# Kernel optimization log

Hardware: AMD Instinct MI355X
Metric: run time of the kernel (lower is better)

Reference implementation:

```python
import jax, jax.numpy as jnp
import numpy as np

MARGIN = 0.2


def _pairwise_distances(emb):
    # Euclidean distances with torch-style zero-masked sqrt (non-squared path).
    dot = jnp.matmul(emb, emb.T)                      # [N, N]
    sq = jnp.diagonal(dot)                            # [N]
    d2 = sq[None, :] - 2.0 * dot + sq[:, None]
    d2 = jnp.maximum(d2, 0.0)
    zero_mask = (d2 == 0.0).astype(d2.dtype)
    return (1.0 - zero_mask) * jnp.sqrt(d2 + zero_mask * 1e-16)


def setup_inputs() -> dict:
    key = jax.random.key(0)
    k1, k2 = jax.random.split(key)
    N, D, C = 512, 512, 64
    labels = jax.random.randint(k1, (N,), 0, C, dtype=jnp.int64 if jax.config.jax_enable_x64 else jnp.int32)
    embeddings = jax.random.normal(k2, (N, D), dtype=jnp.float32)
    return {"labels": labels, "embeddings": embeddings}


def reference(labels, embeddings):
    # Semi-hard... actually Difficulty.Easy path of TripletLoss.forward
    N = embeddings.shape[0]
    pdist = _pairwise_distances(embeddings)                      # [N, N]
    adjacency_not = labels[None, :] != labels[:, None]           # [N, N] bool

    pdist_tile = jnp.tile(pdist, (N, 1))                         # [N*N, N]
    mask = jnp.tile(adjacency_not, (N, 1))                       # [N*N, N]
    # Easy difficulty: negatives strictly farther than the anchor-positive dist
    mask = mask & (pdist_tile > pdist.T.reshape(-1, 1))

    maskf = mask.astype(pdist.dtype)
    mask_final = (jnp.sum(maskf, axis=1, keepdims=True) > 0.0).reshape(N, N).T  # [N, N] bool

    # masked minimum over tiled rows
    axis_max = jnp.max(pdist_tile, axis=1, keepdims=True)
    neg_outside = (jnp.min((pdist_tile - axis_max) * maskf, axis=1, keepdims=True)
                   + axis_max).reshape(N, N).T                   # [N, N]

    # masked maximum over negatives per anchor
    adjf = adjacency_not.astype(pdist.dtype)
    axis_min = jnp.min(pdist, axis=1, keepdims=True)
    neg_inside = jnp.max((pdist - axis_min) * adjf, axis=1, keepdims=True) + axis_min  # [N, 1]
    neg_inside = jnp.broadcast_to(neg_inside, (N, N))

    semi_hard_negatives = jnp.where(mask_final, neg_outside, neg_inside)
    loss_mat = MARGIN + pdist - semi_hard_negatives

    eye = jnp.eye(N, dtype=bool)
    mask_positives = (labels[None, :] == labels[:, None]) & ~eye
    num_positives = jnp.sum(mask_positives).astype(loss_mat.dtype)
    loss = jnp.sum(jnp.maximum(loss_mat * mask_positives.astype(loss_mat.dtype), 0.0))
    return loss / (num_positives + 1e-8)
```

## Files before the change

### kernel.cpp

```cpp
#include <hip/hip_runtime.h>
#include <math.h>


#define NN 512
#define MARGIN_F 0.2f
#define LK 520

typedef __attribute__((ext_vector_type(8))) short bf16x8;
typedef __attribute__((ext_vector_type(4))) float f32x4;

__device__ __forceinline__ unsigned short f2bf(float x){
    unsigned u = __float_as_uint(x);
    return (unsigned short)((u + 0x7FFFu + ((u >> 16) & 1u)) >> 16);
}
__device__ __forceinline__ float bf2f(unsigned short h){
    return __uint_as_float(((unsigned)h) << 16);
}

__global__ __launch_bounds__(256) void k_dist(
    const float* __restrict__ emb,
    float* __restrict__ Dm,
    int* __restrict__ ctrl)
{
    __shared__ __align__(16) char sm[133376];
    short* sh  = (short*)sm;
    float* snI = (float*)(sm + 133120);
    float* snJ = snI + 32;

    const int tid  = threadIdx.x;
    const int wave = tid >> 6, lane = tid & 63;
    const int bi = blockIdx.y, bj = blockIdx.x;

    if (bi == 0 && bj == 0 && tid < 3) ctrl[tid] = 0;

    {
        const int row = tid >> 3;
        const int s8  = tid & 7;
        const float4* Ep = (const float4*)emb;
        float ssI = 0.f, ssJ = 0.f;
        #pragma unroll
        for (int i = 0; i < 16; ++i) {
            const int c4 = s8 + (i << 3);
            const float4 vI = Ep[(size_t)(bi * 32 + row) * 128 + c4];
            const float4 vJ = Ep[(size_t)(bj * 32 + row) * 128 + c4];
            ssI = fmaf(vI.x, vI.x, ssI); ssI = fmaf(vI.y, vI.y, ssI);
            ssI = fmaf(vI.z, vI.z, ssI); ssI = fmaf(vI.w, vI.w, ssI);
            ssJ = fmaf(vJ.x, vJ.x, ssJ); ssJ = fmaf(vJ.y, vJ.y, ssJ);
            ssJ = fmaf(vJ.z, vJ.z, ssJ); ssJ = fmaf(vJ.w, vJ.w, ssJ);
            ushort4 h, l;
            h.x = f2bf(vI.x); l.x = f2bf(vI.x - bf2f(h.x));
            h.y = f2bf(vI.y); l.y = f2bf(vI.y - bf2f(h.y));
            h.z = f2bf(vI.z); l.z = f2bf(vI.z - bf2f(h.z));
            h.w = f2bf(vI.w); l.w = f2bf(vI.w - bf2f(h.w));
            *(ushort4*)(&sh[(0 * 32 + row) * LK + (c4 << 2)]) = h;
            *(ushort4*)(&sh[(1 * 32 + row) * LK + (c4 << 2)]) = l;
            h.x = f2bf(vJ.x); l.x = f2bf(vJ.x - bf2f(h.x));
            h.y = f2bf(vJ.y); l.y = f2bf(vJ.y - bf2f(h.y));
            h.z = f2bf(vJ.z); l.z = f2bf(vJ.z - bf2f(h.z));
            h.w = f2bf(vJ.w); l.w = f2bf(vJ.w - bf2f(h.w));
            *(ushort4*)(&sh[(2 * 32 + row) * LK + (c4 << 2)]) = h;
            *(ushort4*)(&sh[(3 * 32 + row) * LK + (c4 << 2)]) = l;
        }
        ssI += __shfl_xor(ssI, 1, 64); ssJ += __shfl_xor(ssJ, 1, 64);
        ssI += __shfl_xor(ssI, 2, 64); ssJ += __shfl_xor(ssJ, 2, 64);
        ssI += __shfl_xor(ssI, 4, 64); ssJ += __shfl_xor(ssJ, 4, 64);
        if (s8 == 0) { snI[row] = ssI; snJ[row] = ssJ; }
    }
    __syncthreads();

    const int rowb = (wave >> 1) << 4, colb = (wave & 1) << 4;
    const int fr = lane & 15;
    const int k0 = (lane >> 4) << 3;
    f32x4 acc = {0.f, 0.f, 0.f, 0.f};
    #pragma unroll
    for (int t8 = 0; t8 < 16; ++t8) {
        const int k = k0 + (t8 << 5);
        bf16x8 ahi = *(const bf16x8*)(&sh[(0 * 32 + rowb + fr) * LK + k]);
        bf16x8 alo = *(const bf16x8*)(&sh[(1 * 32 + rowb + fr) * LK + k]);
        bf16x8 bhi = *(const bf16x8*)(&sh[(2 * 32 + colb + fr) * LK + k]);
        bf16x8 blo = *(const bf16x8*)(&sh[(3 * 32 + colb + fr) * LK + k]);
        acc = __builtin_amdgcn_mfma_f32_16x16x32_bf16(ahi, bhi, acc, 0, 0, 0);
        acc = __builtin_amdgcn_mfma_f32_16x16x32_bf16(ahi, blo, acc, 0, 0, 0);
        acc = __builtin_amdgcn_mfma_f32_16x16x32_bf16(alo, bhi, acc, 0, 0, 0);
    }
    {
        const int colg = bj * 32 + colb + fr;
        const float sc = snJ[colb + fr];
        const int rl0 = rowb + ((lane >> 4) << 2);
        #pragma unroll
        for (int reg = 0; reg < 4; ++reg) {
            const int rl = rl0 + reg;
            const float d2 = snI[rl] + sc - 2.f * acc[reg];
            Dm[(size_t)(bi * 32 + rl) * NN + colg] = sqrtf(fmaxf(d2, 0.f));
        }
    }
}

__global__ __launch_bounds__(256) void k_mine(
    const int* __restrict__ labels,
    const float* __restrict__ Dm,
    float* __restrict__ accums,
    float* __restrict__ out,
    int nblocks)
{
    __shared__ int slbl[NN];
    __shared__ float drow[4][NN];
    __shared__ unsigned short plist[4][128];
    __shared__ int pcnt[4];

    const int tid = threadIdx.x, wave = tid >> 6, lane = tid & 63;
    const int j = blockIdx.x * 4 + wave;

    slbl[tid] = labels[tid];
    slbl[tid + 256] = labels[tid + 256];
    if (tid < 4) pcnt[tid] = 0;
    __syncthreads();

    const float4* rp = (const float4*)(Dm + (size_t)j * NN);
    const float4 va = rp[lane * 2], vb = rp[lane * 2 + 1];
    *(float4*)(&drow[wave][lane * 8]) = va;
    *(float4*)(&drow[wave][lane * 8 + 4]) = vb;
    float d[8] = {va.x, va.y, va.z, va.w, vb.x, vb.y, vb.z, vb.w};
    const int lj = slbl[j];
    int lb[8];
    #pragma unroll
    for (int m = 0; m < 8; ++m) lb[m] = slbl[lane * 8 + m];

    #pragma unroll
    for (int m = 0; m < 8; ++m){
        const int k = lane * 8 + m;
        if (k != j && lb[m] == lj){
            const int ix = atomicAdd(&pcnt[wave], 1);
            plist[wave][ix] = (unsigned short)k;
        }
    }
    float vmaxl = 0.f;
    #pragma unroll
    for (int m = 0; m < 8; ++m) if (lb[m] != lj) vmaxl = fmaxf(vmaxl, d[m]);
    #pragma unroll
    for (int o = 32; o > 0; o >>= 1) vmaxl = fmaxf(vmaxl, __shfl_xor(vmaxl, o, 64));

    const int np = pcnt[wave];
    float wloss = 0.f;
    for (int p = 0; p < np; ++p){
        const int a = plist[wave][p];
        const float dpa = drow[wave][a];
        float vm = 1e30f;
        #pragma unroll
        for (int m = 0; m < 8; ++m){
            const bool cnd = (lb[m] != lj) && (d[m] > dpa);
            vm = cnd ? fminf(vm, d[m]) : vm;
        }
        #pragma unroll
        for (int o = 32; o > 0; o >>= 1) vm = fminf(vm, __shfl_xor(vm, o, 64));
        const float neg = (vm < 1e29f) ? vm : vmaxl;
        const float term = MARGIN_F + dpa - neg;
        if (lane == 0 && term > 0.f) wloss += term;
    }
    if (lane == 0){
        if (wloss != 0.f) atomicAdd(&accums[0], wloss);
        if (np) atomicAdd((unsigned int*)&accums[1], (unsigned int)np);
    }
    __syncthreads();
    if (tid == 0){
        __threadfence();
        const unsigned old = atomicAdd((unsigned int*)&accums[2], 1u);
        if (old == (unsigned)(nblocks - 1)){
            const float L = atomicAdd(&accums[0], 0.f);
            const unsigned C = atomicAdd((unsigned int*)&accums[1], 0u);
            out[0] = L / ((float)C + 1e-8f);
        }
    }
}

extern "C" void kernel_launch(void* const* d_in, const int* in_sizes, int n_in,
                              void* d_out, int out_size, void* d_ws, size_t ws_size,
                              hipStream_t stream) {
    (void)in_sizes; (void)n_in; (void)out_size; (void)ws_size;
    const int* labels = (const int*)d_in[0];
    const float* emb  = (const float*)d_in[1];
    char* ws = (char*)d_ws;
    float* Dm   = (float*)ws;
    int*   ctrl = (int*)(ws + (1u << 20));

    k_dist<<<dim3(16, 16), 256, 0, stream>>>(emb, Dm, ctrl);
    k_mine<<<128, 256, 0, stream>>>(labels, Dm, (float*)ctrl, (float*)d_out, 128);
}
```

Before: 79.07 us.

## Split K across two wave groups in distance kernel with 512 threads

Doubles the k_dist block to 512 threads. Each thread now loads and splits a single embedding row chunk instead of two, and the MFMA K loop is split between two groups of four waves whose partial accumulators are reduced through shared memory. The LDS row pitch changes from 520 to 528 shorts. The goal is to shorten per-block latency by halving each thread's load and MFMA chain, at the cost of an extra barrier, the scratch reduction, and slightly more shared memory.

```diff
diff --git a/kernel.cpp b/kernel.cpp
--- a/kernel.cpp
+++ b/kernel.cpp
@@ -4,7 +4,7 @@
 
 #define NN 512
 #define MARGIN_F 0.2f
-#define LK 520
+#define LK 528
 
 typedef __attribute__((ext_vector_type(8))) short bf16x8;
 typedef __attribute__((ext_vector_type(4))) float f32x4;
@@ -17,15 +17,22 @@
     return __uint_as_float(((unsigned)h) << 16);
 }
 
-__global__ __launch_bounds__(256) void k_dist(
+#define SH_OFF   0
+#define SNI_OFF  135168
+#define SNJ_OFF  135296
+#define SCR_OFF  135424
+#define SM_BYTES 139520
+
+__global__ __launch_bounds__(512) void k_dist(
     const float* __restrict__ emb,
     float* __restrict__ Dm,
     int* __restrict__ ctrl)
 {
-    __shared__ __align__(16) char sm[133376];
-    short* sh  = (short*)sm;
-    float* snI = (float*)(sm + 133120);
-    float* snJ = snI + 32;
+    __shared__ __align__(16) char sm[SM_BYTES];
+    short* sh  = (short*)(sm + SH_OFF);
+    float* snI = (float*)(sm + SNI_OFF);
+    float* snJ = (float*)(sm + SNJ_OFF);
+    f32x4* scr = (f32x4*)(sm + SCR_OFF);
 
     const int tid  = threadIdx.x;
     const int wave = tid >> 6, lane = tid & 63;
@@ -36,54 +43,55 @@
     {
         const int row = tid >> 3;
         const int s8  = tid & 7;
+        const int isJ = row >> 5;
+        const int rl  = row & 31;
+        const int grow = (isJ ? bj : bi) * 32 + rl;
+        const int bhi = (isJ << 1), blo = bhi + 1;
         const float4* Ep = (const float4*)emb;
-        float ssI = 0.f, ssJ = 0.f;
+        float ss = 0.f;
         #pragma unroll
         for (int i = 0; i < 16; ++i) {
             const int c4 = s8 + (i << 3);
-            const float4 vI = Ep[(size_t)(bi * 32 + row) * 128 + c4];
-            const float4 vJ = Ep[(size_t)(bj * 32 + row) * 128 + c4];
-            ssI = fmaf(vI.x, vI.x, ssI); ssI = fmaf(vI.y, vI.y, ssI);
-            ssI = fmaf(vI.z, vI.z, ssI); ssI = fmaf(vI.w, vI.w, ssI);
-            ssJ = fmaf(vJ.x, vJ.x, ssJ); ssJ = fmaf(vJ.y, vJ.y, ssJ);
-            ssJ = fmaf(vJ.z, vJ.z, ssJ); ssJ = fmaf(vJ.w, vJ.w, ssJ);
+            const float4 v = Ep[(size_t)grow * 128 + c4];
+            ss = fmaf(v.x, v.x, ss); ss = fmaf(v.y, v.y, ss);
+            ss = fmaf(v.z, v.z, ss); ss = fmaf(v.w, v.w, ss);
             ushort4 h, l;
-            h.x = f2bf(vI.x); l.x = f2bf(vI.x - bf2f(h.x));
-            h.y = f2bf(vI.y); l.y = f2bf(vI.y - bf2f(h.y));
-            h.z = f2bf(vI.z); l.z = f2bf(vI.z - bf2f(h.z));
-            h.w = f2bf(vI.w); l.w = f2bf(vI.w - bf2f(h.w));
-            *(ushort4*)(&sh[(0 * 32 + row) * LK + (c4 << 2)]) = h;
-            *(ushort4*)(&sh[(1 * 32 + row) * LK + (c4 << 2)]) = l;
-            h.x = f2bf(vJ.x); l.x = f2bf(vJ.x - bf2f(h.x));
-            h.y = f2bf(vJ.y); l.y = f2bf(vJ.y - bf2f(h.y));
-            h.z = f2bf(vJ.z); l.z = f2bf(vJ.z - bf2f(h.z));
-            h.w = f2bf(vJ.w); l.w = f2bf(vJ.w - bf2f(h.w));
-            *(ushort4*)(&sh[(2 * 32 + row) * LK + (c4 << 2)]) = h;
-            *(ushort4*)(&sh[(3 * 32 + row) * LK + (c4 << 2)]) = l;
+            h.x = f2bf(v.x); l.x = f2bf(v.x - bf2f(h.x));
+            h.y = f2bf(v.y); l.y = f2bf(v.y - bf2f(h.y));
+            h.z = f2bf(v.z); l.z = f2bf(v.z - bf2f(h.z));
+            h.w = f2bf(v.w); l.w = f2bf(v.w - bf2f(h.w));
+            *(ushort4*)(&sh[(bhi * 32 + rl) * LK + (c4 << 2)]) = h;
+            *(ushort4*)(&sh[(blo * 32 + rl) * LK + (c4 << 2)]) = l;
         }
-        ssI += __shfl_xor(ssI, 1, 64); ssJ += __shfl_xor(ssJ, 1, 64);
-        ssI += __shfl_xor(ssI, 2, 64); ssJ += __shfl_xor(ssJ, 2, 64);
-        ssI += __shfl_xor(ssI, 4, 64); ssJ += __shfl_xor(ssJ, 4, 64);
-        if (s8 == 0) { snI[row] = ssI; snJ[row] = ssJ; }
+        ss += __shfl_xor(ss, 1, 64);
+        ss += __shfl_xor(ss, 2, 64);
+        ss += __shfl_xor(ss, 4, 64);
+        if (s8 == 0) { if (isJ) snJ[rl] = ss; else snI[rl] = ss; }
     }
     __syncthreads();
 
-    const int rowb = (wave >> 1) << 4, colb = (wave & 1) << 4;
+    const int quad = wave & 3, khalf = wave >> 2;
+    const int rowb = (quad >> 1) << 4, colb = (quad & 1) << 4;
     const int fr = lane & 15;
     const int k0 = (lane >> 4) << 3;
     f32x4 acc = {0.f, 0.f, 0.f, 0.f};
     #pragma unroll
-    for (int t8 = 0; t8 < 16; ++t8) {
-        const int k = k0 + (t8 << 5);
-        bf16x8 ahi = *(const bf16x8*)(&sh[(0 * 32 + rowb + fr) * LK + k]);
-        bf16x8 alo = *(const bf16x8*)(&sh[(1 * 32 + rowb + fr) * LK + k]);
-        bf16x8 bhi = *(const bf16x8*)(&sh[(2 * 32 + colb + fr) * LK + k]);
-        bf16x8 blo = *(const bf16x8*)(&sh[(3 * 32 + colb + fr) * LK + k]);
+    for (int t8 = 0; t8 < 8; ++t8) {
+        const int k = k0 + (((khalf << 3) + t8) << 5);
+        const bf16x8 ahi = *(const bf16x8*)(&sh[(0 * 32 + rowb + fr) * LK + k]);
+        const bf16x8 alo = *(const bf16x8*)(&sh[(1 * 32 + rowb + fr) * LK + k]);
+        const bf16x8 bhi = *(const bf16x8*)(&sh[(2 * 32 + colb + fr) * LK + k]);
+        const bf16x8 blo = *(const bf16x8*)(&sh[(3 * 32 + colb + fr) * LK + k]);
         acc = __builtin_amdgcn_mfma_f32_16x16x32_bf16(ahi, bhi, acc, 0, 0, 0);
         acc = __builtin_amdgcn_mfma_f32_16x16x32_bf16(ahi, blo, acc, 0, 0, 0);
         acc = __builtin_amdgcn_mfma_f32_16x16x32_bf16(alo, bhi, acc, 0, 0, 0);
     }
-    {
+    if (khalf == 1) scr[quad * 64 + lane] = acc;
+    __syncthreads();
+    if (khalf == 0) {
+        const f32x4 other = scr[quad * 64 + lane];
+        acc[0] += other[0]; acc[1] += other[1];
+        acc[2] += other[2]; acc[3] += other[3];
         const int colg = bj * 32 + colb + fr;
         const float sc = snJ[colb + fr];
         const int rl0 = rowb + ((lane >> 4) << 2);
@@ -183,6 +191,6 @@
     float* Dm   = (float*)ws;
     int*   ctrl = (int*)(ws + (1u << 20));
 
-    k_dist<<<dim3(16, 16), 256, 0, stream>>>(emb, Dm, ctrl);
+    k_dist<<<dim3(16, 16), 512, 0, stream>>>(emb, Dm, ctrl);
     k_mine<<<128, 256, 0, stream>>>(labels, Dm, (float*)ctrl, (float*)d_out, 128);
 }
```

Result: no change. 77.57 us (-1.9%).
